# Performance work log

Hardware: AMD Instinct MI355X
Metric: run time of the kernel (lower is better)

The kernel has to match this reference:

```python
import jax, jax.numpy as jnp
import numpy as np

B, S, C = 2, 4096, 640
HEADS = 10
DH = C // HEADS  # 64
SCALE = 1.0 / np.sqrt(DH).astype(np.float32)


def setup_inputs() -> dict:
    key = jax.random.key(0)
    ks = jax.random.split(key, 5)
    w_std = 0.02
    return {
        "hidden_states": jax.random.normal(ks[0], (B, S, C), dtype=jnp.float32),
        "Wq": jax.random.normal(ks[1], (C, C), dtype=jnp.float32) * w_std,
        "Wk": jax.random.normal(ks[2], (C, C), dtype=jnp.float32) * w_std,
        "Wv": jax.random.normal(ks[3], (C, C), dtype=jnp.float32) * w_std,
        "Wo": jax.random.normal(ks[4], (C, C), dtype=jnp.float32) * w_std,
        "b_out": jnp.zeros((C,), dtype=jnp.float32),
    }


def _split_heads(x):
    # [B, S, C] -> [B, H, S, Dh]
    b, s, c = x.shape
    return x.reshape(b, s, HEADS, DH).transpose(0, 2, 1, 3)


def reference(hidden_states, Wq, Wk, Wv, Wo, b_out):
    residual = hidden_states
    # Linear projections (torch nn.Linear: x @ W.T), to_q/k/v have no bias
    q = jnp.einsum("bsc,dc->bsd", hidden_states, Wq)
    k = jnp.einsum("bsc,dc->bsd", hidden_states, Wk)
    v = jnp.einsum("bsc,dc->bsd", hidden_states, Wv)
    q = _split_heads(q)  # [B, H, S, Dh]
    k = _split_heads(k)
    v = _split_heads(v)
    # get_attention_scores: scaled QK^T + softmax (full O(S^2) matrix)
    scores = jnp.einsum("bhqd,bhkd->bhqk", q, k) * SCALE
    probs = jax.nn.softmax(scores, axis=-1)
    out = jnp.einsum("bhqk,bhkd->bhqd", probs, v)  # [B, H, S, Dh]
    # batch_to_head_dim: [B, H, S, Dh] -> [B, S, C]
    out = out.transpose(0, 2, 1, 3).reshape(hidden_states.shape)
    # to_out[0] Linear (with bias), to_out[1] Dropout = identity at eval
    out = jnp.einsum("bsc,dc->bsd", out, Wo) + b_out
    # residual_connection=True, rescale_output_factor=1.0
    return out + residual
```

## Files before the change

kernel.cpp:

```cpp
#include <hip/hip_runtime.h>
#include <stdint.h>
#include <stddef.h>

#define Bsz 2
#define Ssz 4096
#define Csz 640
#define Hn 10
#define Dh 64
#define NSPLIT 2
#define QROWS 81920

typedef __attribute__((ext_vector_type(8))) short bf16x8;
typedef __attribute__((ext_vector_type(4))) float f32x4;
typedef __attribute__((ext_vector_type(16))) float f32x16;
typedef __attribute__((ext_vector_type(2))) unsigned int u32x2;
typedef __attribute__((ext_vector_type(2))) float f32x2;

typedef __attribute__((address_space(1))) void as1_void;
typedef __attribute__((address_space(3))) void as3_void;

__device__ __forceinline__ void async16(const void* g, void* l) {
  __builtin_amdgcn_global_load_lds((as1_void*)(g), (as3_void*)(l), 16, 0, 0);
}

__device__ __forceinline__ ushort f2bf(float f) {
  union { float f; uint32_t u; } v; v.f = f;
  return (ushort)((v.u + 0x7FFFu + ((v.u >> 16) & 1u)) >> 16);
}

__device__ __forceinline__ uint32_t pack_bf16(float lo, float hi) {
  return __builtin_amdgcn_perm(__float_as_uint(hi), __float_as_uint(lo), 0x07060302u);
}

__device__ __forceinline__ float bf_lo(uint32_t u) {
  return __uint_as_float(u << 16);
}
__device__ __forceinline__ float bf_hi(uint32_t u) {
  return __uint_as_float(u & 0xFFFF0000u);
}

__device__ __forceinline__ float fast_exp2(float x) {
#if __has_builtin(__builtin_amdgcn_exp2f)
  return __builtin_amdgcn_exp2f(x);
#else
  return __exp2f(x);
#endif
}

#define QSCALE 0.1803368801111204f

__global__ __launch_bounds__(256) void cvt_bf16(const float* __restrict__ in,
                                                ushort* __restrict__ out, int n4) {
  int i = blockIdx.x * 256 + threadIdx.x;
  if (i < n4) {
    const float4 v = ((const float4*)in)[i];
    ushort4 o;
    o.x = f2bf(v.x); o.y = f2bf(v.y); o.z = f2bf(v.z); o.w = f2bf(v.w);
    ((ushort4*)out)[i] = o;
  }
}

__global__ __launch_bounds__(256) void cvt4_bf16(
    const float* __restrict__ i0, const float* __restrict__ i1,
    const float* __restrict__ i2, const float* __restrict__ i3,
    ushort* __restrict__ o0, ushort* __restrict__ o1,
    ushort* __restrict__ o2, ushort* __restrict__ o3, int n4) {
  const float* in = (blockIdx.y == 0) ? i0 : (blockIdx.y == 1) ? i1
                    : (blockIdx.y == 2) ? i2 : i3;
  ushort* out = (blockIdx.y == 0) ? o0 : (blockIdx.y == 1) ? o1
                : (blockIdx.y == 2) ? o2 : o3;
  int i = blockIdx.x * 256 + threadIdx.x;
  if (i < n4) {
    const float4 v = ((const float4*)in)[i];
    ushort4 o;
    o.x = f2bf(v.x); o.y = f2bf(v.y); o.z = f2bf(v.z); o.w = f2bf(v.w);
    ((ushort4*)out)[i] = o;
  }
}

template<int MODE>
__global__ __launch_bounds__(256) void gemm_k(
    const ushort* __restrict__ A, const ushort* __restrict__ W0,
    const ushort* __restrict__ W1, const ushort* __restrict__ W2,
    ushort* __restrict__ Qh, ushort* __restrict__ Kh, ushort* __restrict__ Vt,
    const float* __restrict__ bias, const float* __restrict__ residual,
    float* __restrict__ outf)
{
  __shared__ ushort As[128 * 64];
  __shared__ ushort Bs[128 * 64];
  const int t = threadIdx.x;
  const int lane = t & 63;
  const int w = t >> 6;
  const int quad = lane >> 4;
  const int l15 = lane & 15;
  const int m0 = blockIdx.x * 128;
  const int wub = t & ~63;

  int n0, mat;
  const ushort* W;
  if (MODE == 0) {
    mat = blockIdx.y / 5;
    n0 = (blockIdx.y % 5) * 128;
    W = (mat == 0) ? W0 : ((mat == 1) ? W1 : W2);
  } else {
    mat = 0;
    n0 = blockIdx.y * 128;
    W = W0;
  }
  const int qm = (w >> 1) * 64;
  const int qn = (w & 1) * 64;

  f32x4 acc[4][4];
  const f32x4 zero4 = {0.f, 0.f, 0.f, 0.f};
#pragma unroll
  for (int i = 0; i < 4; ++i)
#pragma unroll
    for (int j = 0; j < 4; ++j) acc[i][j] = zero4;

  for (int k0 = 0; k0 < Csz; k0 += 64) {
    __syncthreads();
#pragma unroll
    for (int s = 0; s < 4; ++s) {
      int L = s * 256 + t;
      int row = L >> 3, pc = L & 7;
      int c = pc ^ (row & 7);
      async16(A + (size_t)(m0 + row) * Csz + k0 + c * 8,
              (char*)As + (s * 256 + wub) * 16);
    }
#pragma unroll
    for (int s = 0; s < 4; ++s) {
      int L = s * 256 + t;
      int row = L >> 3, pc = L & 7;
      int c = pc ^ (row & 7);
      async16(W + (size_t)(n0 + row) * Csz + k0 + c * 8,
              (char*)Bs + (s * 256 + wub) * 16);
    }
    __syncthreads();
#pragma unroll
    for (int ks = 0; ks < 2; ++ks) {
      bf16x8 af[4], bfr[4];
#pragma unroll
      for (int i = 0; i < 4; ++i) {
        int row = qm + i * 16 + l15;
        int pc = (ks * 4 + quad) ^ (row & 7);
        af[i] = *(const bf16x8*)(As + row * 64 + pc * 8);
      }
#pragma unroll
      for (int j = 0; j < 4; ++j) {
        int row = qn + j * 16 + l15;
        int pc = (ks * 4 + quad) ^ (row & 7);
        bfr[j] = *(const bf16x8*)(Bs + row * 64 + pc * 8);
      }
#pragma unroll
      for (int i = 0; i < 4; ++i)
#pragma unroll
        for (int j = 0; j < 4; ++j)
          acc[i][j] = __builtin_amdgcn_mfma_f32_16x16x32_bf16(af[i], bfr[j], acc[i][j], 0, 0, 0);
    }
  }

  if (MODE == 0) {
    if (mat < 2) {
      ushort* __restrict__ dst = (mat == 0) ? Qh : Kh;
      const float sc = (mat == 0) ? QSCALE : 1.0f;
#pragma unroll
      for (int j = 0; j < 4; ++j) {
        int n = n0 + qn + j * 16 + l15;
        int h = n >> 6, dh = n & 63;
#pragma unroll
        for (int i = 0; i < 4; ++i) {
#pragma unroll
          for (int r = 0; r < 4; ++r) {
            int m = m0 + qm + i * 16 + quad * 4 + r;
            int b = m >> 12, sidx = m & 4095;
            dst[(((size_t)b * Hn + h) * Ssz + sidx) * Dh + dh] = f2bf(acc[i][j][r] * sc);
          }
        }
      }
    } else {
#pragma unroll
      for (int j = 0; j < 4; ++j) {
        int n = n0 + qn + j * 16 + l15;
        int h = n >> 6, dh = n & 63;
#pragma unroll
        for (int i = 0; i < 4; ++i) {
          int mb = m0 + qm + i * 16 + quad * 4;
          int b = mb >> 12, sidx = mb & 4095;
          ushort4 pk;
          pk.x = f2bf(acc[i][j][0]); pk.y = f2bf(acc[i][j][1]);
          pk.z = f2bf(acc[i][j][2]); pk.w = f2bf(acc[i][j][3]);
          *(ushort4*)(Vt + (((size_t)b * Hn + h) * Dh + dh) * Ssz + sidx) = pk;
        }
      }
    }
  } else {
#pragma unroll
    for (int j = 0; j < 4; ++j) {
      int n = n0 + qn + j * 16 + l15;
      float bs = bias[n];
#pragma unroll
      for (int i = 0; i < 4; ++i) {
#pragma unroll
        for (int r = 0; r < 4; ++r) {
          int m = m0 + qm + i * 16 + quad * 4 + r;
          size_t idx = (size_t)m * Csz + n;
          outf[idx] = acc[i][j][r] + bs + residual[idx];
        }
      }
    }
  }
}

__global__ __launch_bounds__(256, 5) void attn_k(
    const ushort* __restrict__ Qh, const ushort* __restrict__ Kh,
    const ushort* __restrict__ Vt, ushort* __restrict__ Opart,
    float* __restrict__ lpart)
{
  __shared__ ushort Ks[2][64 * 64];
  __shared__ ushort Vs[2][64 * 64];

  const int t = threadIdx.x;
  const int lane = t & 63;
  const int w = t >> 6;
  const int l31 = lane & 31;
  const int hi = lane >> 5;

  const int g = blockIdx.x;
  const int jj = g >> 3;
  const int x = jj & 31;
  const int team = (g & 7) + ((jj >> 5) << 3);
  const int bh = team % 20;
  const int z = team / 20;

  const size_t qk_off = (size_t)bh * Ssz * Dh;
  const size_t v_off = (size_t)bh * Dh * Ssz;
  const int qbase = x * 128 + w * 32;
  const int kvbase = z * (Ssz / NSPLIT);

  bf16x8 qf[4];
  {
    int q = qbase + l31;
#pragma unroll
    for (int ks = 0; ks < 4; ++ks)
      qf[ks] = *(const bf16x8*)(Qh + qk_off + (size_t)q * Dh + ks * 16 + hi * 8);
  }

  f32x16 z16;
#pragma unroll
  for (int i = 0; i < 16; ++i) z16[i] = 0.f;

  f32x16 Oa[2];
  Oa[0] = z16; Oa[1] = z16;
  f32x2 lp2 = {0.f, 0.f};

  int ka[4];
#pragma unroll
  for (int ks = 0; ks < 4; ++ks)
    ka[ks] = l31 * 128 + (((ks * 2 + hi) ^ (l31 & 7)) << 4);

  const int row8 = lane >> 3;
  const int pcs = lane & 7;
#define STAGE(bi, kv)                                                          \
  {                                                                            \
    _Pragma("unroll") for (int s = 0; s < 2; ++s) {                            \
      int i = w * 2 + s;                                                       \
      int row = i * 8 + row8;                                                  \
      int c = pcs ^ (row & 7);                                                 \
      async16(Kh + qk_off + (size_t)(kvbase + (kv) + row) * Dh + c * 8,        \
              (char*)&Ks[bi][0] + i * 1024);                                   \
    }                                                                          \
    _Pragma("unroll") for (int s = 0; s < 2; ++s) {                            \
      int i = w * 2 + s;                                                       \
      int row = i * 8 + row8;                                                  \
      int c = pcs ^ (row & 7);                                                 \
      async16(Vt + v_off + (size_t)row * Ssz + kvbase + (kv) + c * 8,          \
              (char*)&Vs[bi][0] + i * 1024);                                   \
    }                                                                          \
  }

  STAGE(0, 0);

  const char* Kbase = (const char*)&Ks[0][0];
  const char* Vbase = (const char*)&Vs[0][0];

  const int NIT = (Ssz / NSPLIT) / 64;
  for (int it = 0; it < NIT; ++it) {
    const int cb = it & 1;
    asm volatile("s_barrier" ::: "memory");
    if (it + 1 < NIT) {
      STAGE(cb ^ 1, (it + 1) * 64);
      asm volatile("s_waitcnt vmcnt(4)" ::: "memory");
    } else {
      asm volatile("s_waitcnt vmcnt(0)" ::: "memory");
    }
    asm volatile("s_barrier" ::: "memory");

    const int cbo = cb * 8192;

#pragma unroll
    for (int tau = 0; tau < 2; ++tau) {
      f32x16 Sq;
#pragma unroll
      for (int ks = 0; ks < 4; ++ks) {
        bf16x8 kf = *(const bf16x8*)(Kbase + cbo + tau * 4096 + ka[ks]);
        Sq = __builtin_amdgcn_mfma_f32_32x32x16_bf16(kf, qf[ks],
                                                     ks == 0 ? z16 : Sq, 0, 0, 0);
      }
      uint32_t pk[8];
#pragma unroll
      for (int a = 0; a < 8; ++a) {
        float p0 = fast_exp2(Sq[2 * a]);
        float p1 = fast_exp2(Sq[2 * a + 1]);
        f32x2 pp = {p0, p1};
        lp2 += pp;
        pk[a] = pack_bf16(p0, p1);
      }

#pragma unroll
      for (int k2 = 0; k2 < 2; ++k2) {
        const int ks2 = tau * 2 + k2;
        const int bA = (2 * ks2) & 3;
        const int bB = (2 * ks2 + 1) & 3;
        u32x2 r0 = __builtin_amdgcn_permlane32_swap(pk[2 * bA],
                                                    pk[2 * bB], false, false);
        u32x2 r1 = __builtin_amdgcn_permlane32_swap(pk[2 * bA + 1],
                                                    pk[2 * bB + 1], false, false);
        union { uint32_t u[4]; bf16x8 v; } pu;
        pu.u[0] = r0.x; pu.u[1] = r1.x;
        pu.u[2] = r0.y; pu.u[3] = r1.y;
        bf16x8 pf = pu.v;
#pragma unroll
        for (int mt = 0; mt < 2; ++mt) {
          bf16x8 vfr = *(const bf16x8*)(Vbase + cbo + mt * 4096 + ka[ks2]);
          Oa[mt] = __builtin_amdgcn_mfma_f32_32x32x16_bf16(vfr, pf, Oa[mt], 0, 0, 0);
        }
      }
    }
  }
#undef STAGE

  const size_t prow_base = (size_t)z * QROWS + (size_t)bh * Ssz;
  float l_part = lp2.x + lp2.y;
  float l_tot = l_part + __shfl_xor(l_part, 32, 64);
  int q = qbase + l31;
  if (hi == 0) lpart[prow_base + q] = l_tot;
  ushort* dst = Opart + (prow_base + q) * 64;
#pragma unroll
  for (int mt = 0; mt < 2; ++mt) {
#pragma unroll
    for (int gg = 0; gg < 4; ++gg) {
      int dh0 = mt * 32 + 8 * gg + 4 * hi;
      uint2 val;
      val.x = pack_bf16(Oa[mt][4 * gg + 0], Oa[mt][4 * gg + 1]);
      val.y = pack_bf16(Oa[mt][4 * gg + 2], Oa[mt][4 * gg + 3]);
      *(uint2*)(dst + dh0) = val;
    }
  }
}

__global__ __launch_bounds__(256) void combine_k(
    const ushort* __restrict__ Opart, const float* __restrict__ lpart,
    ushort* __restrict__ attnb)
{
  int gid = blockIdx.x * 256 + threadIdx.x;
  int row = gid >> 4;
  int dh0 = (gid & 15) * 4;
  int bh = row >> 12, q = row & 4095;
  int b = bh / Hn, h = bh % Hn;
  float a0 = 0.f, a1 = 0.f, a2 = 0.f, a3 = 0.f, lsum = 0.f;
#pragma unroll
  for (int sp = 0; sp < NSPLIT; ++sp) {
    uint2 v = *(const uint2*)(Opart + ((size_t)sp * QROWS + row) * 64 + dh0);
    a0 += bf_lo(v.x); a1 += bf_hi(v.x);
    a2 += bf_lo(v.y); a3 += bf_hi(v.y);
    lsum += lpart[(size_t)sp * QROWS + row];
  }
  float inv = 1.0f / lsum;
  uint2 o;
  o.x = pack_bf16(a0 * inv, a1 * inv);
  o.y = pack_bf16(a2 * inv, a3 * inv);
  *(uint2*)(attnb + ((size_t)b * Ssz + q) * Csz + h * Dh + dh0) = o;
}

extern "C" void kernel_launch(void* const* d_in, const int* in_sizes, int n_in,
                              void* d_out, int out_size, void* d_ws, size_t ws_size,
                              hipStream_t stream) {
  (void)in_sizes; (void)n_in; (void)out_size; (void)ws_size;
  const float* hs = (const float*)d_in[0];
  const float* Wq = (const float*)d_in[1];
  const float* Wk = (const float*)d_in[2];
  const float* Wv = (const float*)d_in[3];
  const float* Wo = (const float*)d_in[4];
  const float* bo = (const float*)d_in[5];
  float* out = (float*)d_out;

  char* ws = (char*)d_ws;
  ushort* Xbf = (ushort*)(ws);
  ushort* Wqb = (ushort*)(ws + 10485760);
  ushort* Wkb = (ushort*)(ws + 10485760 + 819200);
  ushort* Wvb = (ushort*)(ws + 10485760 + 2 * 819200);
  ushort* Wob = (ushort*)(ws + 10485760 + 3 * 819200);
  ushort* Qh  = (ushort*)(ws + 13762560);
  ushort* Kh  = (ushort*)(ws + 13762560 + 10485760);
  ushort* Vt  = (ushort*)(ws + 13762560 + 2 * 10485760);
  ushort* attnb = (ushort*)(ws + 13762560 + 3 * 10485760);
  ushort* Opart = (ushort*)(ws + 55705600);
  float*  lpart = (float*)(ws + 55705600 + 41943040);

  hipLaunchKernelGGL(cvt_bf16, dim3(5120), dim3(256), 0, stream, hs, Xbf, 1310720);
  hipLaunchKernelGGL(cvt4_bf16, dim3(400, 4), dim3(256), 0, stream,
                     Wq, Wk, Wv, Wo, Wqb, Wkb, Wvb, Wob, 102400);

  hipLaunchKernelGGL((gemm_k<0>), dim3(64, 15), dim3(256), 0, stream,
                     Xbf, Wqb, Wkb, Wvb, Qh, Kh, Vt, (const float*)nullptr,
                     (const float*)nullptr, (float*)nullptr);
  hipLaunchKernelGGL(attn_k, dim3(32 * 20 * NSPLIT), dim3(256), 0, stream,
                     Qh, Kh, Vt, Opart, lpart);
  hipLaunchKernelGGL(combine_k, dim3(QROWS / 16), dim3(256), 0, stream,
                     Opart, lpart, attnb);
  hipLaunchKernelGGL((gemm_k<1>), dim3(64, 5), dim3(256), 0, stream,
                     attnb, Wob, (const ushort*)nullptr, (const ushort*)nullptr,
                     (ushort*)nullptr, (ushort*)nullptr, (ushort*)nullptr,
                     bo, hs, out);
}
```

Before: 242.7 us.

## Single-buffer V in attention and stage K and V loads at separate points

The attention kernel now keeps K double-buffered in LDS but V single-buffered, cutting LDS per block. The next K tile is prefetched at the start of each iteration. The next V tile is loaded after the PV MFMAs finish, and the QK^T plus exp stage of the following iteration hides that load. QK^T for both halves now runs before the PV loop, with barriers rearranged to match. The trade-off is an extra full vmcnt(0) wait and barrier per iteration, and V latency is hidden only by the QK stage.

```diff
diff --git a/kernel.cpp b/kernel.cpp
--- a/kernel.cpp
+++ b/kernel.cpp
@@ -217,7 +217,7 @@
     float* __restrict__ lpart)
 {
   __shared__ ushort Ks[2][64 * 64];
-  __shared__ ushort Vs[2][64 * 64];
+  __shared__ ushort Vs[64 * 64];
 
   const int t = threadIdx.x;
   const int lane = t & 63;
@@ -260,43 +260,43 @@
 
   const int row8 = lane >> 3;
   const int pcs = lane & 7;
-#define STAGE(bi, kv)                                                          \
+#define STAGE_K(bi, kv)                                                        \
   {                                                                            \
     _Pragma("unroll") for (int s = 0; s < 2; ++s) {                            \
       int i = w * 2 + s;                                                       \
       int row = i * 8 + row8;                                                  \
       int c = pcs ^ (row & 7);                                                 \
       async16(Kh + qk_off + (size_t)(kvbase + (kv) + row) * Dh + c * 8,        \
-              (char*)&Ks[bi][0] + i * 1024);                                   \
+              (char*)&Ks[0][0] + (bi) * 8192 + i * 1024);                      \
     }                                                                          \
+  }
+#define STAGE_V(kv)                                                            \
+  {                                                                            \
     _Pragma("unroll") for (int s = 0; s < 2; ++s) {                            \
       int i = w * 2 + s;                                                       \
       int row = i * 8 + row8;                                                  \
       int c = pcs ^ (row & 7);                                                 \
       async16(Vt + v_off + (size_t)row * Ssz + kvbase + (kv) + c * 8,          \
-              (char*)&Vs[bi][0] + i * 1024);                                   \
+              (char*)&Vs[0] + i * 1024);                                       \
     }                                                                          \
   }
 
-  STAGE(0, 0);
+  STAGE_K(0, 0);
+  STAGE_V(0);
+  asm volatile("s_waitcnt vmcnt(0)" ::: "memory");
+  asm volatile("s_barrier" ::: "memory");
 
   const char* Kbase = (const char*)&Ks[0][0];
-  const char* Vbase = (const char*)&Vs[0][0];
+  const char* Vbase = (const char*)&Vs[0];
 
   const int NIT = (Ssz / NSPLIT) / 64;
   for (int it = 0; it < NIT; ++it) {
     const int cb = it & 1;
-    asm volatile("s_barrier" ::: "memory");
-    if (it + 1 < NIT) {
-      STAGE(cb ^ 1, (it + 1) * 64);
-      asm volatile("s_waitcnt vmcnt(4)" ::: "memory");
-    } else {
-      asm volatile("s_waitcnt vmcnt(0)" ::: "memory");
-    }
-    asm volatile("s_barrier" ::: "memory");
-
     const int cbo = cb * 8192;
 
+    if (it + 1 < NIT) STAGE_K(cb ^ 1, (it + 1) * 64);
+
+    uint32_t pk[2][8];
 #pragma unroll
     for (int tau = 0; tau < 2; ++tau) {
       f32x16 Sq;
@@ -306,38 +306,51 @@
         Sq = __builtin_amdgcn_mfma_f32_32x32x16_bf16(kf, qf[ks],
                                                      ks == 0 ? z16 : Sq, 0, 0, 0);
       }
-      uint32_t pk[8];
 #pragma unroll
       for (int a = 0; a < 8; ++a) {
         float p0 = fast_exp2(Sq[2 * a]);
         float p1 = fast_exp2(Sq[2 * a + 1]);
         f32x2 pp = {p0, p1};
         lp2 += pp;
-        pk[a] = pack_bf16(p0, p1);
-      }
-
-#pragma unroll
-      for (int k2 = 0; k2 < 2; ++k2) {
-        const int ks2 = tau * 2 + k2;
-        const int bA = (2 * ks2) & 3;
-        const int bB = (2 * ks2 + 1) & 3;
-        u32x2 r0 = __builtin_amdgcn_permlane32_swap(pk[2 * bA],
-                                                    pk[2 * bB], false, false);
-        u32x2 r1 = __builtin_amdgcn_permlane32_swap(pk[2 * bA + 1],
-                                                    pk[2 * bB + 1], false, false);
-        union { uint32_t u[4]; bf16x8 v; } pu;
-        pu.u[0] = r0.x; pu.u[1] = r1.x;
-        pu.u[2] = r0.y; pu.u[3] = r1.y;
-        bf16x8 pf = pu.v;
-#pragma unroll
-        for (int mt = 0; mt < 2; ++mt) {
-          bf16x8 vfr = *(const bf16x8*)(Vbase + cbo + mt * 4096 + ka[ks2]);
-          Oa[mt] = __builtin_amdgcn_mfma_f32_32x32x16_bf16(vfr, pf, Oa[mt], 0, 0, 0);
-        }
-      }
-    }
-  }
-#undef STAGE
+        pk[tau][a] = pack_bf16(p0, p1);
+      }
+    }
+
+    if (it + 1 < NIT) {
+      asm volatile("s_waitcnt vmcnt(2)" ::: "memory");
+    } else {
+      asm volatile("s_waitcnt vmcnt(0)" ::: "memory");
+    }
+    asm volatile("s_barrier" ::: "memory");
+
+#pragma unroll
+    for (int ks2 = 0; ks2 < 4; ++ks2) {
+      const int ts = ks2 >> 1;
+      const int bA = (2 * ks2) & 3;
+      const int bB = (2 * ks2 + 1) & 3;
+      u32x2 r0 = __builtin_amdgcn_permlane32_swap(pk[ts][2 * bA],
+                                                  pk[ts][2 * bB], false, false);
+      u32x2 r1 = __builtin_amdgcn_permlane32_swap(pk[ts][2 * bA + 1],
+                                                  pk[ts][2 * bB + 1], false, false);
+      union { uint32_t u[4]; bf16x8 v; } pu;
+      pu.u[0] = r0.x; pu.u[1] = r1.x;
+      pu.u[2] = r0.y; pu.u[3] = r1.y;
+      bf16x8 pf = pu.v;
+#pragma unroll
+      for (int mt = 0; mt < 2; ++mt) {
+        bf16x8 vfr = *(const bf16x8*)(Vbase + mt * 4096 + ka[ks2]);
+        Oa[mt] = __builtin_amdgcn_mfma_f32_32x32x16_bf16(vfr, pf, Oa[mt], 0, 0, 0);
+      }
+    }
+
+    if (it + 1 < NIT) {
+      asm volatile("s_waitcnt vmcnt(0)" ::: "memory");
+      asm volatile("s_barrier" ::: "memory");
+      STAGE_V((it + 1) * 64);
+    }
+  }
+#undef STAGE_K
+#undef STAGE_V
 
   const size_t prow_base = (size_t)z * QROWS + (size_t)bh * Ssz;
   float l_part = lp2.x + lp2.y;
```

New measurement: 251.3 us. 1.04x slower.
